# Kernel optimization log

Hardware: AMD Instinct MI355X
Metric: run time of the kernel (lower is better)

The kernel has to match this reference:

```python
import jax, jax.numpy as jnp
import numpy as np

EPS = 1e-05
PC_RANGE = (-61.2, -61.2, -10.0, 61.2, 61.2, 10.0)


def _grid_sample_points(feat, gx, gy):
    """Bilinear grid_sample (align_corners=False, zeros padding) at one point per query.
    feat: (BN, C, H, W); gx, gy: (BN, M) normalized coords in [-1, 1].
    Returns (BN, C, M)."""
    BN, C, H, W = feat.shape
    x = (gx + 1.0) * (W * 0.5) - 0.5
    y = (gy + 1.0) * (H * 0.5) - 0.5
    x0 = jnp.floor(x)
    y0 = jnp.floor(y)
    x1 = x0 + 1.0
    y1 = y0 + 1.0
    wx1 = x - x0
    wx0 = 1.0 - wx1
    wy1 = y - y0
    wy0 = 1.0 - wy1
    feat_flat = feat.reshape(BN, C, H * W)

    def gather(xi, yi):
        valid = (xi >= 0) & (xi < W) & (yi >= 0) & (yi < H)
        xc = jnp.clip(xi, 0, W - 1).astype(jnp.int32)
        yc = jnp.clip(yi, 0, H - 1).astype(jnp.int32)
        idx = yc * W + xc  # (BN, M)
        v = jnp.take_along_axis(feat_flat, idx[:, None, :], axis=2)  # (BN, C, M)
        return v * valid[:, None, :].astype(feat.dtype)

    out = (gather(x0, y0) * (wx0 * wy0)[:, None, :]
           + gather(x1, y0) * (wx1 * wy0)[:, None, :]
           + gather(x0, y1) * (wx0 * wy1)[:, None, :]
           + gather(x1, y1) * (wx1 * wy1)[:, None, :])
    return out


def setup_inputs() -> dict:
    key = jax.random.key(0)
    ks = jax.random.split(key, 6)
    B, N, C, M = 2, 6, 256, 900
    shapes = [(116, 200), (58, 100), (29, 50), (15, 25)]
    feats = [jax.random.normal(ks[i], (B, N, C, h, w), dtype=jnp.float32)
             for i, (h, w) in enumerate(shapes)]
    reference_points = jax.random.uniform(ks[4], (B, M, 3), dtype=jnp.float32)
    lidar2img = jax.random.normal(ks[5], (B, N, 4, 4), dtype=jnp.float32)
    return {"feat0": feats[0], "feat1": feats[1], "feat2": feats[2], "feat3": feats[3],
            "reference_points": reference_points, "lidar2img": lidar2img}


def reference(feat0, feat1, feat2, feat3, reference_points, lidar2img):
    features = [feat0, feat1, feat2, feat3]
    B, M, _ = reference_points.shape
    N = lidar2img.shape[1]
    # denormalize reference points into the point-cloud range
    scale = jnp.array([PC_RANGE[3] - PC_RANGE[0], PC_RANGE[4] - PC_RANGE[1], PC_RANGE[5] - PC_RANGE[2]], dtype=reference_points.dtype)
    offset = jnp.array([PC_RANGE[0], PC_RANGE[1], PC_RANGE[2]], dtype=reference_points.dtype)
    ref_3d = reference_points * scale + offset  # (B, M, 3)
    ref_homo = jnp.concatenate([ref_3d, jnp.ones_like(ref_3d[..., :1])], axis=-1)  # (B, M, 4)
    # project: (B, N, M, 4)
    cam = jnp.einsum('bnij,bmj->bnmi', lidar2img, ref_homo)
    z = cam[..., 2]
    valid = (z > EPS).astype(cam.dtype)  # (B, N, M)
    px = cam[..., 0] / (z + EPS)  # (B, N, M)
    py = cam[..., 1] / (z + EPS)

    lvl_samples = []
    for feat in features:
        _, _, C, H, W = feat.shape
        gx = (px / W) * 2.0 - 1.0
        gy = (py / H) * 2.0 - 1.0
        samp = _grid_sample_points(feat.reshape(B * N, C, H, W),
                                   gx.reshape(B * N, M), gy.reshape(B * N, M))  # (BN, C, M)
        samp = samp.reshape(B, N, C, M).transpose(0, 3, 1, 2)  # (B, M, N, C)
        lvl_samples.append(samp)
    sampled = jnp.stack(lvl_samples, axis=0).mean(axis=0)  # (B, M, N, C)

    mask = valid.transpose(0, 2, 1)[..., None]  # (B, M, N, 1)
    out = (sampled * mask).sum(axis=2) / (mask.sum(axis=2) + EPS)  # (B, M, C)
    return out
```

## Files before the change

### kernel.cpp

```cpp
#include <hip/hip_runtime.h>


static constexpr float EPSV = 1e-5f;
static constexpr int Bn = 2, Nn = 6, Cn = 256, Mn = 900;

__global__ __launch_bounds__(256) void FeatureSampler_74062416052404_kernel(
    const float* __restrict__ f0, const float* __restrict__ f1,
    const float* __restrict__ f2, const float* __restrict__ f3,
    const float* __restrict__ refp, const float* __restrict__ l2i,
    float* __restrict__ out)
{
    const int bm = blockIdx.x;
    const int b  = bm / Mn;
    const int m  = bm - b * Mn;
    const int c  = threadIdx.x;

    const float rx = refp[(b * Mn + m) * 3 + 0] * 122.4f - 61.2f;
    const float ry = refp[(b * Mn + m) * 3 + 1] * 122.4f - 61.2f;
    const float rz = refp[(b * Mn + m) * 3 + 2] * 20.0f  - 10.0f;

    const float* const feats[4] = {f0, f1, f2, f3};
    constexpr int Hs[4] = {116, 58, 29, 15};
    constexpr int Ws[4] = {200, 100, 50, 25};

    float acc  = 0.0f;
    float wsum = 0.0f;

    for (int n = 0; n < Nn; ++n) {
        const float* L = l2i + (size_t)(b * Nn + n) * 16;
        const float cx = L[0] * rx + L[1] * ry + L[2]  * rz + L[3];
        const float cy = L[4] * rx + L[5] * ry + L[6]  * rz + L[7];
        const float cz = L[8] * rx + L[9] * ry + L[10] * rz + L[11];

        if (!(cz > EPSV)) continue;
        wsum += 1.0f;

        const float inv = 1.0f / (cz + EPSV);
        const float x   = cx * inv - 0.5f;
        const float y   = cy * inv - 0.5f;
        const float x0f = floorf(x);
        const float y0f = floorf(y);
        const float x1f = x0f + 1.0f;
        const float y1f = y0f + 1.0f;
        const float wx1 = x - x0f, wx0 = 1.0f - wx1;
        const float wy1 = y - y0f, wy0 = 1.0f - wy1;

#pragma unroll
        for (int l = 0; l < 4; ++l) {
            const int H = Hs[l], W = Ws[l];
            const bool vx0 = (x0f >= 0.0f) & (x0f < (float)W);
            const bool vx1 = (x1f >= 0.0f) & (x1f < (float)W);
            const bool vy0 = (y0f >= 0.0f) & (y0f < (float)H);
            const bool vy1 = (y1f >= 0.0f) & (y1f < (float)H);
            if (!((vx0 | vx1) & (vy0 | vy1))) continue;

            const int xi0 = (int)x0f;
            const int yi0 = (int)y0f;
            const float* base =
                feats[l] + (size_t)((b * Nn + n) * Cn + c) * (H * W);

            float s = 0.0f;
            if (vx0 & vy0) s += wx0 * wy0 * base[yi0 * W + xi0];
            if (vx1 & vy0) s += wx1 * wy0 * base[yi0 * W + xi0 + 1];
            if (vx0 & vy1) s += wx0 * wy1 * base[(yi0 + 1) * W + xi0];
            if (vx1 & vy1) s += wx1 * wy1 * base[(yi0 + 1) * W + xi0 + 1];
            acc += s;
        }
    }

    out[(size_t)(b * Mn + m) * Cn + c] = acc * 0.25f / (wsum + EPSV);
}

extern "C" void kernel_launch(void* const* d_in, const int* in_sizes, int n_in,
                              void* d_out, int out_size, void* d_ws, size_t ws_size,
                              hipStream_t stream) {
    const float* f0   = (const float*)d_in[0];
    const float* f1   = (const float*)d_in[1];
    const float* f2   = (const float*)d_in[2];
    const float* f3   = (const float*)d_in[3];
    const float* refp = (const float*)d_in[4];
    const float* l2i  = (const float*)d_in[5];
    float* out = (float*)d_out;

    dim3 grid(Bn * Mn);
    dim3 block(256);
    FeatureSampler_74062416052404_kernel<<<grid, block, 0, stream>>>(
        f0, f1, f2, f3, refp, l2i, out);
}
```

Measured before the change: 390.6 us.

## Transpose features to channel-last fp16 before coalesced bilinear gather

Adds a per-call tiled transpose that converts each feature level from NCHW fp32 into an NHWC fp16 workspace. The sampling kernel then reads the four corner pixels as contiguous channel vectors, two channels per thread, so loads are coalesced instead of scattered across channel planes. The cost is an extra full pass over all feature maps, about 380MB of reads plus half-size writes, on every call. Storing features as fp16 also adds rounding error.

```diff
diff --git a/kernel.cpp b/kernel.cpp
--- a/kernel.cpp
+++ b/kernel.cpp
@@ -1,29 +1,89 @@
 #include <hip/hip_runtime.h>
+#include <hip/hip_fp16.h>
 
 
 static constexpr float EPSV = 1e-5f;
 static constexpr int Bn = 2, Nn = 6, Cn = 256, Mn = 900;
 
+static constexpr int H0=116, W0=200, HW0=H0*W0;
+static constexpr int H1= 58, W1=100, HW1=H1*W1;
+static constexpr int H2= 29, W2= 50, HW2=H2*W2;
+static constexpr int H3= 15, W3= 25, HW3=H3*W3;
+
+static constexpr size_t OFF0 = 0;
+static constexpr size_t OFF1 = OFF0 + (size_t)Bn*Nn*HW0*Cn;
+static constexpr size_t OFF2 = OFF1 + (size_t)Bn*Nn*HW1*Cn;
+static constexpr size_t OFF3 = OFF2 + (size_t)Bn*Nn*HW2*Cn;
+
+struct alignas(8) Half4 { __half2 a, b; };
+
+template<bool VEC>
+__global__ __launch_bounds__(256) void transpose_kernel(
+    const float* __restrict__ in, __half* __restrict__ outT, int HW)
+{
+    __shared__ float tile[64][68];
+    const int t   = threadIdx.x;
+    const int hw0 = blockIdx.x * 64;
+    const int c0  = blockIdx.y * 64;
+    const int bn  = blockIdx.z;
+    const float* src = in + ((size_t)bn * Cn + c0) * HW;
+
+    if (VEC) {
+        const int hwi = (t & 15) * 4;
+        const int cr  = t >> 4;
+#pragma unroll
+        for (int i = 0; i < 4; ++i) {
+            const int c = cr + i * 16;
+            if (hw0 + hwi < HW) {
+                const float4 v = *(const float4*)(src + (size_t)c * HW + hw0 + hwi);
+                *(float4*)&tile[c][hwi] = v;
+            }
+        }
+    } else {
+        const int lane = t & 63;
+        const int cr   = t >> 6;
+#pragma unroll
+        for (int i = 0; i < 16; ++i) {
+            const int c = cr + i * 4;
+            if (hw0 + lane < HW)
+                tile[c][lane] = src[(size_t)c * HW + hw0 + lane];
+        }
+    }
+    __syncthreads();
+
+    const int cq = (t & 15) * 4;
+    const int r0 = t >> 4;
+#pragma unroll
+    for (int i = 0; i < 4; ++i) {
+        const int row = r0 + i * 16;
+        if (hw0 + row < HW) {
+            Half4 h;
+            h.a = __floats2half2_rn(tile[cq+0][row], tile[cq+1][row]);
+            h.b = __floats2half2_rn(tile[cq+2][row], tile[cq+3][row]);
+            *(Half4*)(outT + ((size_t)bn * HW + hw0 + row) * Cn + c0 + cq) = h;
+        }
+    }
+}
+
 __global__ __launch_bounds__(256) void FeatureSampler_74062416052404_kernel(
-    const float* __restrict__ f0, const float* __restrict__ f1,
-    const float* __restrict__ f2, const float* __restrict__ f3,
+    const __half* __restrict__ ws,
     const float* __restrict__ refp, const float* __restrict__ l2i,
     float* __restrict__ out)
 {
-    const int bm = blockIdx.x;
-    const int b  = bm / Mn;
-    const int m  = bm - b * Mn;
-    const int c  = threadIdx.x;
+    const int q = blockIdx.x * 2 + threadIdx.y;
+    const int b = q / Mn;
+    const int m = q - b * Mn;
+    const int c = threadIdx.x * 2;
 
-    const float rx = refp[(b * Mn + m) * 3 + 0] * 122.4f - 61.2f;
-    const float ry = refp[(b * Mn + m) * 3 + 1] * 122.4f - 61.2f;
-    const float rz = refp[(b * Mn + m) * 3 + 2] * 20.0f  - 10.0f;
+    const float rx = refp[q * 3 + 0] * 122.4f - 61.2f;
+    const float ry = refp[q * 3 + 1] * 122.4f - 61.2f;
+    const float rz = refp[q * 3 + 2] * 20.0f  - 10.0f;
 
-    const float* const feats[4] = {f0, f1, f2, f3};
-    constexpr int Hs[4] = {116, 58, 29, 15};
-    constexpr int Ws[4] = {200, 100, 50, 25};
+    const __half* T[4] = { ws + OFF0, ws + OFF1, ws + OFF2, ws + OFF3 };
+    constexpr int Hs[4] = {H0, H1, H2, H3};
+    constexpr int Ws_[4] = {W0, W1, W2, W3};
 
-    float acc  = 0.0f;
+    float ax = 0.0f, ay = 0.0f;
     float wsum = 0.0f;
 
     for (int n = 0; n < Nn; ++n) {
@@ -31,44 +91,54 @@
         const float cx = L[0] * rx + L[1] * ry + L[2]  * rz + L[3];
         const float cy = L[4] * rx + L[5] * ry + L[6]  * rz + L[7];
         const float cz = L[8] * rx + L[9] * ry + L[10] * rz + L[11];
-
         if (!(cz > EPSV)) continue;
         wsum += 1.0f;
 
         const float inv = 1.0f / (cz + EPSV);
-        const float x   = cx * inv - 0.5f;
-        const float y   = cy * inv - 0.5f;
-        const float x0f = floorf(x);
-        const float y0f = floorf(y);
-        const float x1f = x0f + 1.0f;
-        const float y1f = y0f + 1.0f;
+        const float x = cx * inv - 0.5f;
+        const float y = cy * inv - 0.5f;
+        const float x0f = floorf(x), y0f = floorf(y);
         const float wx1 = x - x0f, wx0 = 1.0f - wx1;
         const float wy1 = y - y0f, wy0 = 1.0f - wy1;
 
 #pragma unroll
         for (int l = 0; l < 4; ++l) {
-            const int H = Hs[l], W = Ws[l];
+            const int H = Hs[l], W = Ws_[l];
             const bool vx0 = (x0f >= 0.0f) & (x0f < (float)W);
-            const bool vx1 = (x1f >= 0.0f) & (x1f < (float)W);
+            const bool vx1 = (x0f >= -1.0f) & (x0f < (float)(W - 1));
             const bool vy0 = (y0f >= 0.0f) & (y0f < (float)H);
-            const bool vy1 = (y1f >= 0.0f) & (y1f < (float)H);
+            const bool vy1 = (y0f >= -1.0f) & (y0f < (float)(H - 1));
             if (!((vx0 | vx1) & (vy0 | vy1))) continue;
 
             const int xi0 = (int)x0f;
             const int yi0 = (int)y0f;
-            const float* base =
-                feats[l] + (size_t)((b * Nn + n) * Cn + c) * (H * W);
+            const __half* base = T[l]
+                + ((size_t)((b * Nn + n) * (size_t)(H * W)) + (size_t)yi0 * W + xi0) * Cn + c;
 
-            float s = 0.0f;
-            if (vx0 & vy0) s += wx0 * wy0 * base[yi0 * W + xi0];
-            if (vx1 & vy0) s += wx1 * wy0 * base[yi0 * W + xi0 + 1];
-            if (vx0 & vy1) s += wx0 * wy1 * base[(yi0 + 1) * W + xi0];
-            if (vx1 & vy1) s += wx1 * wy1 * base[(yi0 + 1) * W + xi0 + 1];
-            acc += s;
+            float sx = 0.0f, sy = 0.0f;
+            if (vx0 & vy0) {
+                const float2 v = __half22float2(*(const __half2*)(base));
+                sx += wx0 * wy0 * v.x;  sy += wx0 * wy0 * v.y;
+            }
+            if (vx1 & vy0) {
+                const float2 v = __half22float2(*(const __half2*)(base + Cn));
+                sx += wx1 * wy0 * v.x;  sy += wx1 * wy0 * v.y;
+            }
+            if (vx0 & vy1) {
+                const float2 v = __half22float2(*(const __half2*)(base + (size_t)W * Cn));
+                sx += wx0 * wy1 * v.x;  sy += wx0 * wy1 * v.y;
+            }
+            if (vx1 & vy1) {
+                const float2 v = __half22float2(*(const __half2*)(base + (size_t)W * Cn + Cn));
+                sx += wx1 * wy1 * v.x;  sy += wx1 * wy1 * v.y;
+            }
+            ax += sx;  ay += sy;
         }
     }
 
-    out[(size_t)(b * Mn + m) * Cn + c] = acc * 0.25f / (wsum + EPSV);
+    const float scale = 0.25f / (wsum + EPSV);
+    float2 r;  r.x = ax * scale;  r.y = ay * scale;
+    *(float2*)(out + (size_t)q * Cn + c) = r;
 }
 
 extern "C" void kernel_launch(void* const* d_in, const int* in_sizes, int n_in,
@@ -81,9 +151,13 @@
     const float* refp = (const float*)d_in[4];
     const float* l2i  = (const float*)d_in[5];
     float* out = (float*)d_out;
+    __half* ws = (__half*)d_ws;
 
-    dim3 grid(Bn * Mn);
-    dim3 block(256);
-    FeatureSampler_74062416052404_kernel<<<grid, block, 0, stream>>>(
-        f0, f1, f2, f3, refp, l2i, out);
+    transpose_kernel<true ><<<dim3((HW0 + 63) / 64, 4, Bn * Nn), 256, 0, stream>>>(f0, ws + OFF0, HW0);
+    transpose_kernel<true ><<<dim3((HW1 + 63) / 64, 4, Bn * Nn), 256, 0, stream>>>(f1, ws + OFF1, HW1);
+    transpose_kernel<false><<<dim3((HW2 + 63) / 64, 4, Bn * Nn), 256, 0, stream>>>(f2, ws + OFF2, HW2);
+    transpose_kernel<false><<<dim3((HW3 + 63) / 64, 4, Bn * Nn), 256, 0, stream>>>(f3, ws + OFF3, HW3);
+
+    FeatureSampler_74062416052404_kernel<<<dim3(Bn * Mn / 2), dim3(128, 2), 0, stream>>>(
+        ws, refp, l2i, out);
 }
```

Measured after the change: 483.7 us. 23.8% more time.
